# Kernel optimization log

Measured on AMD Instinct MI355X. Metric: run time of the kernel, lower is better.

The kernel has to match this reference:

```python
import jax, jax.numpy as jnp
import numpy as np

E, H, O = 300, 256, 2            # embedding_size, hidden_size, output_size
N_SENT, SENT_LEN, CLAIM_LEN = 2048, 64, 64


def setup_inputs() -> dict:
    key = jax.random.key(0)
    ks = jax.random.split(key, 24)
    rn = lambda k, shape, s=0.05: (jax.random.normal(k, shape, jnp.float32) * s)
    return {
        "claim": jax.random.normal(ks[0], (CLAIM_LEN, E), jnp.float32),
        "sentences": jax.random.normal(ks[1], (N_SENT, SENT_LEN, E), jnp.float32),
        # claim GRU (PyTorch layout: W_ih (3H,E), W_hh (3H,H), gates ordered r,z,n)
        "Wih_c": rn(ks[2], (3 * H, E)), "Whh_c": rn(ks[3], (3 * H, H)),
        "bih_c": rn(ks[4], (3 * H,)), "bhh_c": rn(ks[5], (3 * H,)),
        # sentence GRU
        "Wih_s": rn(ks[6], (3 * H, E)), "Whh_s": rn(ks[7], (3 * H, H)),
        "bih_s": rn(ks[8], (3 * H,)), "bhh_s": rn(ks[9], (3 * H,)),
        # gates (no bias)
        "Wg_s": rn(ks[10], (1, H)), "Wg_c": rn(ks[11], (1, H)),
        # coherence attention
        "Wac": rn(ks[12], (H, H)), "bac": rn(ks[13], (H,)),
        "Was": rn(ks[14], (1, H)), "bas": rn(ks[15], (1,)),
        # extension linear (H, 2H)
        "Wext": rn(ks[16], (H, 2 * H)), "bext": rn(ks[17], (H,)),
        # joint linear (H, 4H), no bias
        "Wj": rn(ks[18], (H, 4 * H)),
        # entailment attention
        "Wae": rn(ks[19], (1, H)), "bae": rn(ks[20], (1,)),
        # final classifier
        "Wf": rn(ks[21], (O, H)), "bf": rn(ks[22], (O,)),
    }


def _gru_last(x, Wih, Whh, bih, bhh):
    """x: (T, B, E) -> final hidden state (B, H). PyTorch GRU math, zero init."""
    B = x.shape[1]
    Hd = Whh.shape[1]
    gi = jnp.einsum('tbe,ge->tbg', x, Wih) + bih  # (T, B, 3H), input projections

    def step(h, gi_t):
        gh = h @ Whh.T + bhh
        ir, iz, inn = jnp.split(gi_t, 3, axis=-1)
        hr, hz, hn = jnp.split(gh, 3, axis=-1)
        r = jax.nn.sigmoid(ir + hr)
        z = jax.nn.sigmoid(iz + hz)
        n = jnp.tanh(inn + r * hn)
        return (1.0 - z) * n + z * h, None

    h0 = jnp.zeros((B, Hd), x.dtype)
    hT, _ = jax.lax.scan(step, h0, gi)
    return hT


def reference(claim, sentences, Wih_c, Whh_c, bih_c, bhh_c,
              Wih_s, Whh_s, bih_s, bhh_s, Wg_s, Wg_c,
              Wac, bac, Was, bas, Wext, bext, Wj, Wae, bae, Wf, bf):
    # claim encoder: (T,1,E) -> hc (1,H)
    hc = _gru_last(claim[:, None, :], Wih_c, Whh_c, bih_c, bhh_c)
    # batched sentence encoder (replaces the per-sentence Python loop)
    HS = _gru_last(jnp.transpose(sentences, (1, 0, 2)), Wih_s, Whh_s, bih_s, bhh_s)  # (N,H)
    # gated fusion of sentence reps with claim rep
    g = jax.nn.sigmoid(HS @ Wg_s.T + hc @ Wg_c.T)          # (N,1)
    HSg = g * HS + (1.0 - g) * hc                           # (N,H)
    # coherence attention over sentences (row-wise softmax)
    scores = (HSg @ Wac.T + bac) @ HSg.T + (HSg @ Was.T + bas)  # (N,N)
    coh = jax.nn.softmax(scores, axis=1)
    H_apo = coh @ HSg                                       # (N,H)
    H_tilde = jnp.tanh(jnp.concatenate([HS, H_apo], axis=1) @ Wext.T + bext)  # (N,H)
    # joint claim-sentence entailment features (replaces per-row loop)
    hc_b = jnp.broadcast_to(hc, H_tilde.shape)
    joint_in = jnp.concatenate(
        [hc_b, H_tilde, hc * H_tilde, jnp.abs(hc - H_tilde)], axis=1)  # (N,4H)
    H_c_s = jnp.tanh(joint_in @ Wj.T)                       # (N,H)
    # entailment attention (softmax over sentence axis)
    ae = jnp.tanh(H_c_s @ Wae.T + bae)                      # (N,1)
    w = jax.nn.softmax(ae, axis=0)                          # (N,1)
    h_c_S = w.T @ H_c_s                                     # (1,H)
    return jax.nn.sigmoid(h_c_S @ Wf.T + bf)                # (1,O)
```

## Files before the change

### kernel.cpp

```cpp
#include <hip/hip_runtime.h>

typedef unsigned short u16;
typedef unsigned int u32;
typedef short bf16x8 __attribute__((ext_vector_type(8)));
typedef float f32x4 __attribute__((ext_vector_type(4)));
typedef u16 u16x4v __attribute__((ext_vector_type(4)));

__device__ __forceinline__ float b2f(u16 h){ return __uint_as_float(((unsigned)h)<<16); }
__device__ __forceinline__ u16 f2b(float f){
  unsigned u = __float_as_uint(f);
  u += 0x7fffu + ((u>>16)&1u);
  return (u16)(u>>16);
}
__device__ __forceinline__ float sigm(float x){ return 1.f/(1.f+__expf(-x)); }
__device__ __forceinline__ float tanh_(float x){
  float ax=fabsf(x), e=__expf(-2.f*ax), t=(1.f-e)/(1.f+e);
  return x<0.f? -t : t;
}
__device__ __forceinline__ bf16x8 ld8a(const u16* p){
  union{ u16x4v h[2]; bf16x8 v; } u;
  u.h[0]=*(const u16x4v*)p; u.h[1]=*(const u16x4v*)(p+4); return u.v;
}
__device__ __forceinline__ f32x4 mfma16(bf16x8 a, bf16x8 b, f32x4 c){
  return __builtin_amdgcn_mfma_f32_16x16x32_bf16(a,b,c,0,0,0);
}

__device__ __forceinline__ void gl_lds16(const void* g, void* s){
  __builtin_amdgcn_global_load_lds(
      (const __attribute__((address_space(1))) void*)g,
      (__attribute__((address_space(3))) void*)s, 16, 0, 0);
}

__device__ __forceinline__ void stage_rows(const u16* base, int ld, int kc,
                                           u16* buf, int w, int l){
  #pragma unroll
  for (int ii=0; ii<6; ii++){
    const int i   = w + ii*8;
    const int row = i*16 + (l>>2);
    const int c8  = (l&3) ^ ((row>>2)&3);
    gl_lds16(base + (long)row*ld + kc*32 + c8*8, buf + i*512);
  }
}
__device__ __forceinline__ bf16x8 ldB(const u16* buf, int row, int l){
  const int slot = (l>>4) ^ ((row>>2)&3);
  return *(const bf16x8*)((const char*)buf + row*64 + slot*16);
}

__global__ __launch_bounds__(256) void cvt_kernel(
    const float* __restrict__ WihS, const float* __restrict__ WhhS,
    const float* __restrict__ WihC, const float* __restrict__ WhhC,
    const float* __restrict__ Wac,  const float* __restrict__ Wext,
    const float* __restrict__ Wj,
    const float* __restrict__ bihS, const float* __restrict__ bhhS,
    const float* __restrict__ bihC, const float* __restrict__ bhhC,
    u16* __restrict__ WihP, u16* __restrict__ WhhSb,
    u16* __restrict__ WihCP, u16* __restrict__ WhhCb,
    u16* __restrict__ WacB, u16* __restrict__ WextB, u16* __restrict__ WjB,
    float* __restrict__ biasGI, float* __restrict__ biasGIC)
{
  const int seg = blockIdx.y;
  int n;
  switch(seg){
    case 0: n = 768*320; break;  case 1: n = 196608; break;
    case 2: n = 768*320; break;  case 3: n = 196608; break;
    case 4: n = 65536; break;    case 5: n = 131072; break;
    case 6: n = 262144; break;   default: n = 1536; break;
  }
  for (int i = blockIdx.x*256 + threadIdx.x; i < n; i += gridDim.x*256){
    switch(seg){
      case 0: { int r=i/320, c=i-r*320; WihP[i]  = (c<300)? f2b(WihS[r*300+c]) : (u16)0; } break;
      case 1: WhhSb[i] = f2b(WhhS[i]); break;
      case 2: { int r=i/320, c=i-r*320; WihCP[i] = (c<300)? f2b(WihC[r*300+c]) : (u16)0; } break;
      case 3: WhhCb[i] = f2b(WhhC[i]); break;
      case 4: WacB[i]  = f2b(Wac[i]);  break;
      case 5: WextB[i] = f2b(Wext[i]); break;
      case 6: WjB[i]   = f2b(Wj[i]);   break;
      default:
        if (i < 768) biasGI[i] = bihS[i] + (i < 512 ? bhhS[i] : 0.f);
        else { int j = i - 768; biasGIC[j] = bihC[j] + (j < 512 ? bhhC[j] : 0.f); }
        break;
    }
  }
}

__global__ __launch_bounds__(512) void gi_kernel(
    const int pass,
    const float* __restrict__ sents, const float* __restrict__ claim,
    const u16* __restrict__ WihP, const float* __restrict__ biasGI,
    const u16* __restrict__ WihCP, const float* __restrict__ biasGIC,
    u16* __restrict__ gi_b, float* __restrict__ giC)
{
  __shared__ __align__(16) u16 SA[64*320];
  __shared__ __align__(16) u16 BB[2][768*32];
  const int tid=threadIdx.x, w=tid>>6, l=tid&63, ar=l&15, kg8=(l>>4)*8;
  const f32x4 z4 = {0.f,0.f,0.f,0.f};
  const bool isClaim = (blockIdx.x == 1024);
  const int b = blockIdx.x;

  for (int i=tid; i<64*80; i+=512){
    int r = i/80, q = i - r*80;
    u16x4v o;
    if (q < 75){
      float4 v;
      if (!isClaim) v = ((const float4*)sents)[(long)(2*b + (r>>5))*4800 + (pass*32 + (r&31))*75 + q];
      else          v = ((const float4*)claim)[r*75 + q];
      o[0]=f2b(v.x); o[1]=f2b(v.y); o[2]=f2b(v.z); o[3]=f2b(v.w);
    } else { o[0]=0; o[1]=0; o[2]=0; o[3]=0; }
    int byte = r*640 + q*8; byte ^= (r&7)<<4;
    *(u16x4v*)((char*)SA + byte) = o;
  }
  const u16* Bw = isClaim ? WihCP : WihP;
  stage_rows(Bw, 320, 0, BB[0], w, l);
  __syncthreads();

  f32x4 acc[24];
  #pragma unroll
  for (int q=0;q<24;q++) acc[q]=z4;

  int cur = 0;
  #pragma unroll
  for (int kc=0;kc<10;kc++){
    if (kc < 9) stage_rows(Bw, 320, kc+1, BB[cur^1], w, l);
    bf16x8 bq[6];
    #pragma unroll
    for (int q=0;q<6;q++) bq[q] = ldB(BB[cur], w*96 + q*16 + ar, l);
    #pragma unroll
    for (int m=0;m<4;m++){
      const int abyte = ((m*16+ar)*640 + (kc*32+kg8)*2) ^ ((ar&7)<<4);
      const bf16x8 a = *(const bf16x8*)((const char*)SA + abyte);
      #pragma unroll
      for (int q=0;q<6;q++) acc[m*6+q] = mfma16(a, bq[q], acc[m*6+q]);
    }
    __syncthreads();
    cur ^= 1;
  }
  const int rb = (l>>4)*4;
  if (!isClaim){
    #pragma unroll
    for (int q=0;q<6;q++){
      const int c = w*96 + q*16 + ar;
      const float bs = biasGI[c];
      #pragma unroll
      for (int m=0;m<4;m++)
        #pragma unroll
        for (int p=0;p<4;p++)
          gi_b[(long)(b*64 + m*16 + rb + p)*768 + c] = f2b(acc[m*6+q][p] + bs);
    }
  } else {
    #pragma unroll
    for (int q=0;q<6;q++){
      const int c = w*96 + q*16 + ar;
      const float bs = biasGIC[c];
      #pragma unroll
      for (int m=0;m<4;m++)
        #pragma unroll
        for (int p=0;p<4;p++)
          giC[(m*16 + rb + p)*768 + c] = acc[m*6+q][p] + bs;
    }
  }
}

__global__ __launch_bounds__(512) void rec_kernel(
    const int pass,
    const u16* __restrict__ gi_b, const u16* __restrict__ WhhSb,
    const float* __restrict__ bhhS,
    float* __restrict__ Hmid, u16* __restrict__ HSout,
    const float* __restrict__ giC, const u16* __restrict__ WhhCb,
    const float* __restrict__ bhhC, const float* __restrict__ Wj,
    const float* __restrict__ WgC,
    float* __restrict__ hcMid, float* __restrict__ hcf,
    float* __restrict__ cvec, float* __restrict__ c0p)
{
  __shared__ __align__(16) u16 Hb[2][16][256];
  __shared__ __align__(16) u16 giL[2][8][776];
  __shared__ __align__(16) u16 WB[2][768*32];
  __shared__ float ghL[768];
  __shared__ float hfL[256];
  __shared__ __align__(16) u16 hbL[256];
  const int tid=threadIdx.x, w=tid>>6, l=tid&63, ar=l&15, kg8=(l>>4)*8;
  const f32x4 z4 = {0.f,0.f,0.f,0.f};

  if (blockIdx.x != 0){
    const long i0 = (long)(blockIdx.x - 1)*8;
    const int rb = (l>>4)*4;
    const float bhn0 = bhhS[512 + w*32 +  0 + ar];
    const float bhn1 = bhhS[512 + w*32 + 16 + ar];

    for (int i=tid; i<2*16*256; i+=512) ((u16*)Hb)[i] = 0;
    __syncthreads();
    float hold[2][4];
    #pragma unroll
    for (int ti=0;ti<2;ti++)
      #pragma unroll
      for (int p=0;p<4;p++) hold[ti][p] = 0.f;
    if (pass==1 && l<32){
      #pragma unroll
      for (int ti=0;ti<2;ti++){
        #pragma unroll
        for (int p=0;p<4;p++){
          const int c = w*32 + ti*16 + ar, rr = rb + p;
          const float h = Hmid[(i0+rr)*256 + c];
          hold[ti][p] = h;
          const int byte = (rr*512 + c*2) ^ ((rr&7)<<4);
          *(u16*)((char*)&Hb[0][0][0] + byte) = f2b(h);
        }
      }
    }
    const u32* g32 = (const u32*)gi_b;
    u32 pf[6];
    #pragma unroll
    for (int rep=0;rep<6;rep++){
      const int i = rep*512 + tid, j = i/384, cu = i - j*384;
      pf[rep] = g32[((i0+j)*32 + 0)*384 + cu];
    }
    #pragma unroll
    for (int rep=0;rep<6;rep++){
      const int i = rep*512 + tid, j = i/384, cu = i - j*384;
      *(u32*)((char*)&giL[0][0][0] + j*1552 + cu*4) = pf[rep];
    }
    stage_rows(WhhSb, 256, 0, WB[0], w, l);
    __syncthreads();

    int cur = 0, kb = 0;
    for (int tl=0; tl<32; tl++){
      const int tn = (tl<31) ? tl+1 : 31;
      #pragma unroll
      for (int rep=0;rep<6;rep++){
        const int i = rep*512 + tid, j = i/384, cu = i - j*384;
        pf[rep] = g32[((i0+j)*32 + tn)*384 + cu];
      }
      f32x4 acc[6];
      #pragma unroll
      for (int q=0;q<6;q++) acc[q]=z4;
      if (l < 32){
        #pragma unroll
        for (int s=0;s<2;s++)
          #pragma unroll
          for (int ti=0;ti<2;ti++)
            #pragma unroll
            for (int p=0;p<4;p++){
              const int c = w*32 + ti*16 + ar;
              const u16 v = *(const u16*)((const char*)&giL[cur][0][0] + (rb+p)*1552 + (s*256+c)*2);
              acc[s*2+ti][p] = b2f(v);
            }
      }
      #pragma unroll
      for (int kc=0;kc<8;kc++){
        const int nkc = (kc<7) ? kc+1 : 0;
        stage_rows(WhhSb, 256, nkc, WB[kb^1], w, l);
        const int abyte = (ar*512 + (kc*32+kg8)*2) ^ ((ar&7)<<4);
        const bf16x8 a = *(const bf16x8*)((const char*)&Hb[cur][0][0] + abyte);
        bf16x8 wq[6];
        #pragma unroll
        for (int s=0;s<3;s++)
          #pragma unroll
          for (int ti=0;ti<2;ti++)
            wq[s*2+ti] = ldB(WB[kb], s*256 + w*32 + ti*16 + ar, l);
        #pragma unroll
        for (int q=0;q<6;q++) acc[q] = mfma16(a, wq[q], acc[q]);
        __syncthreads();
        kb ^= 1;
      }
      #pragma unroll
      for (int rep=0;rep<6;rep++){
        const int i = rep*512 + tid, j = i/384, cu = i - j*384;
        *(u32*)((char*)&giL[cur^1][0][0] + j*1552 + cu*4) = pf[rep];
      }
      if (l < 32){
        #pragma unroll
        for (int ti=0;ti<2;ti++){
          const int c = w*32 + ti*16 + ar;
          const float bhn = ti ? bhn1 : bhn0;
          #pragma unroll
          for (int p=0;p<4;p++){
            const int rr = rb + p;
            const u16 gv = *(const u16*)((const char*)&giL[cur][0][0] + rr*1552 + (512+c)*2);
            const float r_ = sigm(acc[0+ti][p]);
            const float z_ = sigm(acc[2+ti][p]);
            const float n_ = tanh_(b2f(gv) + r_*(acc[4+ti][p] + bhn));
            const float h = (1.f - z_)*n_ + z_*hold[ti][p];
            hold[ti][p] = h;
            const int byte = (rr*512 + c*2) ^ ((rr&7)<<4);
            *(u16*)((char*)&Hb[cur^1][0][0] + byte) = f2b(h);
          }
        }
      }
      __syncthreads();
      cur ^= 1;
    }
    if (l < 32){
      #pragma unroll
      for (int ti=0;ti<2;ti++){
        #pragma unroll
        for (int p=0;p<4;p++){
          const int c = w*32 + ti*16 + ar, rr = rb + p;
          if (pass==0) Hmid[(i0+rr)*256 + c] = hold[ti][p];
          else         HSout[(i0+rr)*512 + c] = f2b(hold[ti][p]);
        }
      }
    }
  } else {
    const u16* wrow[6];
    #pragma unroll
    for (int q=0;q<6;q++) wrow[q] = WhhCb + (w*96 + q*16 + ar)*256 + kg8;
    if (tid < 256){
      const float h0 = (pass==0) ? 0.f : hcMid[tid];
      hfL[tid] = h0; hbL[tid] = f2b(h0);
    }
    __syncthreads();
    for (int tl=0; tl<32; tl++){
      const int t = pass*32 + tl;
      f32x4 a6[6];
      #pragma unroll
      for (int q=0;q<6;q++) a6[q]=z4;
      #pragma unroll
      for (int kc=0;kc<8;kc++){
        bf16x8 wq[6];
        #pragma unroll
        for (int q=0;q<6;q++) wq[q] = ld8a(wrow[q] + kc*32);
        const bf16x8 a = ld8a((const u16*)hbL + kc*32 + kg8);
        #pragma unroll
        for (int q=0;q<6;q++) a6[q] = mfma16(a, wq[q], a6[q]);
      }
      if (l < 16){
        #pragma unroll
        for (int q=0;q<6;q++) ghL[w*96 + q*16 + l] = a6[q][0];
      }
      __syncthreads();
      if (tid < 256){
        const int c = tid;
        const float r_ = sigm(giC[t*768 +       c] + ghL[c]);
        const float z_ = sigm(giC[t*768 + 256 + c] + ghL[256 + c]);
        const float n_ = tanh_(giC[t*768 + 512 + c] + r_*(ghL[512 + c] + bhhC[512 + c]));
        const float h = (1.f - z_)*n_ + z_*hfL[c];
        hfL[c] = h; hbL[c] = f2b(h);
      }
      __syncthreads();
    }
    if (tid < 256){
      const int c = tid;
      const float hv = hfL[c];
      if (pass == 0) hcMid[c] = hv;
      else {
        hcf[c] = hv;
        float acc2 = 0.f;
        for (int k=0;k<256;k++) acc2 += hfL[k]*Wj[(long)c*1024 + k];
        cvec[c] = acc2;
        if (c==0){ float s=0.f; for (int k=0;k<256;k++) s += hfL[k]*WgC[k]; *c0p = s; }
      }
    }
  }
}

__global__ __launch_bounds__(256) void fusion_kernel(
    const u16* __restrict__ HSH, const float* __restrict__ Wgs,
    const float* __restrict__ hcf, const float* __restrict__ c0p,
    u16* __restrict__ HSg, u16* __restrict__ HSgT)
{
  __shared__ float gbuf[64];
  __shared__ __align__(16) u16 tile[64][258];
  const int tid=threadIdx.x, w=tid>>6, l=tid&63;
  const long i0 = (long)blockIdx.x * 64;
  const float c0 = *c0p;
  for (int rr=0; rr<16; rr++){
    long i = i0 + w*16 + rr;
    float p = 0.f;
    for (int c=l; c<256; c+=64) p += b2f(HSH[i*512+c]) * Wgs[c];
    for (int o=32;o;o>>=1) p += __shfl_down(p,o,64);
    if (l==0) gbuf[w*16+rr] = sigm(p + c0);
  }
  __syncthreads();
  for (int idx=tid; idx<64*256; idx+=256){
    int r = idx>>8, c = idx&255;
    float g = gbuf[r];
    float hs = b2f(HSH[(i0+r)*512 + c]);
    u16 bv = f2b(g*hs + (1.f-g)*hcf[c]);
    HSg[(i0+r)*256 + c] = bv;
    tile[r][c] = bv;
  }
  __syncthreads();
  const int ioff = tid&63, cg = tid>>6;
  for (int cc=cg; cc<256; cc+=4)
    HSgT[(long)cc*2048 + i0 + ioff] = tile[ioff][cc];
}

template<int MODE>
__global__ __launch_bounds__(256) void gemmk(
    const u16* __restrict__ A, long lda,
    const u16* __restrict__ Bw, long ldb,
    void* __restrict__ Cp, long ldc, int K,
    const float* __restrict__ biasf,
    const float* __restrict__ hc)
{
  const int tid=threadIdx.x, w=tid>>6, l=tid&63, ar=l&15, kg8=(l>>4)*8;
  const long row0 = (long)blockIdx.x*64 + w*16;
  const long col0 = (long)blockIdx.y*64;
  const f32x4 z4 = {0.f,0.f,0.f,0.f};
  f32x4 acc[4] = {z4,z4,z4,z4};
  const u16* ap = A + (row0+ar)*lda + kg8;
  const u16* bp0 = Bw + (col0+ 0+ar)*ldb + kg8;
  const u16* bp1 = Bw + (col0+16+ar)*ldb + kg8;
  const u16* bp2 = Bw + (col0+32+ar)*ldb + kg8;
  const u16* bp3 = Bw + (col0+48+ar)*ldb + kg8;
  for (int k0=0; k0<K; k0+=32){
    bf16x8 a = ld8a(ap + k0);
    acc[0] = mfma16(a, ld8a(bp0+k0), acc[0]);
    acc[1] = mfma16(a, ld8a(bp1+k0), acc[1]);
    acc[2] = mfma16(a, ld8a(bp2+k0), acc[2]);
    acc[3] = mfma16(a, ld8a(bp3+k0), acc[3]);
  }
  const int rbase = (l>>4)*4;
  #pragma unroll
  for (int t=0;t<4;t++){
    long c = col0 + t*16 + ar;
    #pragma unroll
    for (int p=0;p<4;p++){
      long r = row0 + rbase + p;
      float v = acc[t][p];
      if constexpr (MODE==0){
        if (biasf) v += biasf[c];
        ((u16*)Cp)[r*ldc + c] = f2b(v);
      } else if constexpr (MODE==1){
        ((float*)Cp)[r*ldc + c] = v;
      } else if constexpr (MODE==2){
        float tv = tanh_(v + biasf[c]);
        u16* Uo = (u16*)Cp;
        float hv = hc[c];
        Uo[r*768 + c]       = f2b(tv);
        Uo[r*768 + 256 + c] = f2b(hv*tv);
        Uo[r*768 + 512 + c] = f2b(fabsf(hv - tv));
      } else {
        float tv = tanh_(v + biasf[c]);
        ((u16*)Cp)[r*ldc + c] = f2b(tv);
      }
    }
  }
}

__global__ __launch_bounds__(256) void softmax_rows(float* __restrict__ S)
{
  __shared__ float buf[2048];
  __shared__ float red[4];
  const long i = blockIdx.x;
  float* row = S + i*2048;
  const int tid = threadIdx.x;
  float m = -1e30f;
  for (int c=tid; c<2048; c+=256){ float v=row[c]; buf[c]=v; m=fmaxf(m,v); }
  for (int o=32;o;o>>=1) m = fmaxf(m, __shfl_down(m,o,64));
  if ((tid&63)==0) red[tid>>6] = m;
  __syncthreads();
  m = fmaxf(fmaxf(red[0],red[1]), fmaxf(red[2],red[3]));
  __syncthreads();
  float s = 0.f;
  for (int c=tid; c<2048; c+=256){ float e=__expf(buf[c]-m); buf[c]=e; s+=e; }
  for (int o=32;o;o>>=1) s += __shfl_down(s,o,64);
  if ((tid&63)==0) red[tid>>6] = s;
  __syncthreads();
  s = red[0]+red[1]+red[2]+red[3];
  const float rinv = 1.f/s;
  u16* P = (u16*)S + i*4096;
  for (int c=tid; c<2048; c+=256) P[c] = f2b(buf[c]*rinv);
}

__global__ __launch_bounds__(256) void ae_kernel(
    const u16* __restrict__ Hcs, const float* __restrict__ Wae, const float* __restrict__ bae,
    float* __restrict__ part, float* __restrict__ psum)
{
  __shared__ float aebuf[64];
  const int b=blockIdx.x, tid=threadIdx.x, w=tid>>6, l=tid&63;
  const long i0 = (long)b*64;
  const float baev = bae[0];
  for (int rr=0; rr<16; rr++){
    long i = i0 + w*16 + rr;
    float p = 0.f;
    for (int c=l; c<256; c+=64) p += b2f(Hcs[i*256+c]) * Wae[c];
    for (int o=32;o;o>>=1) p += __shfl_down(p,o,64);
    if (l==0) aebuf[w*16+rr] = __expf(tanh_(p + baev));
  }
  __syncthreads();
  float acc = 0.f;
  const int c = tid;
  for (int r=0;r<64;r++) acc += aebuf[r] * b2f(Hcs[(i0+r)*256 + c]);
  part[b*256 + c] = acc;
  if (tid==0){ float s=0.f; for (int r=0;r<64;r++) s+=aebuf[r]; psum[b]=s; }
}

__global__ __launch_bounds__(256) void final_kernel(
    const float* __restrict__ part, const float* __restrict__ psum,
    const float* __restrict__ Wf, const float* __restrict__ bf_, float* __restrict__ out)
{
  __shared__ float hbuf[256];
  __shared__ float ssum;
  const int tid = threadIdx.x;
  float v = 0.f;
  for (int b=0;b<32;b++) v += part[b*256 + tid];
  hbuf[tid] = v;
  if (tid==0){ float s=0.f; for (int b=0;b<32;b++) s+=psum[b]; ssum=s; }
  __syncthreads();
  const int w = tid>>6, l = tid&63;
  if (w < 2){
    float rinv = 1.f/ssum;
    float p = 0.f;
    for (int c=l; c<256; c+=64) p += hbuf[c]*rinv*Wf[w*256 + c];
    for (int o=32;o;o>>=1) p += __shfl_down(p,o,64);
    if (l==0) out[w] = sigm(p + bf_[w]);
  }
}

extern "C" void kernel_launch(void* const* d_in, const int* in_sizes, int n_in,
                              void* d_out, int out_size, void* d_ws, size_t ws_size,
                              hipStream_t stream)
{
  const float* claim=(const float*)d_in[0];
  const float* sents=(const float*)d_in[1];
  const float* WihC =(const float*)d_in[2];
  const float* WhhC =(const float*)d_in[3];
  const float* bihC =(const float*)d_in[4];
  const float* bhhC =(const float*)d_in[5];
  const float* WihS =(const float*)d_in[6];
  const float* WhhS =(const float*)d_in[7];
  const float* bihS =(const float*)d_in[8];
  const float* bhhS =(const float*)d_in[9];
  const float* WgS  =(const float*)d_in[10];
  const float* WgC  =(const float*)d_in[11];
  const float* Wac  =(const float*)d_in[12];
  const float* bac  =(const float*)d_in[13];
  const float* Wext =(const float*)d_in[16];
  const float* bext =(const float*)d_in[17];
  const float* Wj   =(const float*)d_in[18];
  const float* Wae  =(const float*)d_in[19];
  const float* bae  =(const float*)d_in[20];
  const float* Wf   =(const float*)d_in[21];
  const float* bf_  =(const float*)d_in[22];

  char* ws = (char*)d_ws;
  size_t off = 0;
  auto alloc = [&](size_t b)->void*{ void* p = ws + off; off = (off + b + 255) & ~(size_t)255; return p; };
  float* hcf  = (float*)alloc(256*4);
  float* cvec = (float*)alloc(256*4);
  float* c0p  = (float*)alloc(16);
  float* hcMid= (float*)alloc(256*4);
  float* giC  = (float*)alloc((size_t)64*768*4);
  u16* WihP   = (u16*)alloc((size_t)768*320*2);
  u16* WhhSb  = (u16*)alloc((size_t)196608*2);
  u16* WihCP  = (u16*)alloc((size_t)768*320*2);
  u16* WhhCb  = (u16*)alloc((size_t)196608*2);
  u16* WacB   = (u16*)alloc((size_t)65536*2);
  u16* WextB  = (u16*)alloc((size_t)131072*2);
  u16* WjB    = (u16*)alloc((size_t)262144*2);
  float* biasGI  = (float*)alloc(768*4);
  float* biasGIC = (float*)alloc(768*4);
  u16* HSH  = (u16*)alloc((size_t)2048*512*2);
  u16* HSg  = (u16*)alloc((size_t)2048*256*2);
  u16* HSgT = (u16*)alloc((size_t)256*2048*2);
  u16* A1   = (u16*)alloc((size_t)2048*256*2);
  u16* Up   = (u16*)alloc((size_t)2048*768*2);
  u16* Hcs  = (u16*)alloc((size_t)2048*256*2);
  float* part = (float*)alloc(32*256*4);
  float* psum = (float*)alloc(32*4);
  float* Hmid = (float*)alloc((size_t)2048*256*4);
  u16* gi_b   = (u16*)alloc((size_t)65536*768*2);
  float* S    = (float*)gi_b;

  cvt_kernel<<<dim3(960,8),256,0,stream>>>(WihS,WhhS,WihC,WhhC,Wac,Wext,Wj,
                                           bihS,bhhS,bihC,bhhC,
                                           WihP,WhhSb,WihCP,WhhCb,WacB,WextB,WjB,
                                           biasGI,biasGIC);
  gi_kernel<<<1025,512,0,stream>>>(0,sents,claim,WihP,biasGI,WihCP,biasGIC,gi_b,giC);
  rec_kernel<<<257,512,0,stream>>>(0,gi_b,WhhSb,bhhS,Hmid,HSH,
                                   giC,WhhCb,bhhC,Wj,WgC,hcMid,hcf,cvec,c0p);
  gi_kernel<<<1024,512,0,stream>>>(1,sents,claim,WihP,biasGI,WihCP,biasGIC,gi_b,giC);
  rec_kernel<<<257,512,0,stream>>>(1,gi_b,WhhSb,bhhS,Hmid,HSH,
                                   giC,WhhCb,bhhC,Wj,WgC,hcMid,hcf,cvec,c0p);

  fusion_kernel<<<32,256,0,stream>>>(HSH,WgS,hcf,c0p,HSg,HSgT);
  gemmk<0><<<dim3(32,4),256,0,stream>>>(HSg,256L,WacB,256L,(void*)A1,256L,256,bac,nullptr);
  gemmk<1><<<dim3(32,32),256,0,stream>>>(A1,256L,HSg,256L,(void*)S,2048L,256,nullptr,nullptr);
  softmax_rows<<<2048,256,0,stream>>>(S);
  gemmk<0><<<dim3(32,4),256,0,stream>>>((const u16*)S,4096L,HSgT,2048L,(void*)(HSH+256),512L,2048,nullptr,nullptr);
  gemmk<2><<<dim3(32,4),256,0,stream>>>(HSH,512L,WextB,512L,(void*)Up,768L,512,bext,hcf);
  gemmk<3><<<dim3(32,4),256,0,stream>>>(Up,768L,WjB+256,1024L,(void*)Hcs,256L,768,cvec,nullptr);
  ae_kernel<<<32,256,0,stream>>>(Hcs,Wae,bae,part,psum);
  final_kernel<<<1,256,0,stream>>>(part,psum,Wf,bf_,(float*)d_out);
}
```

Measured before the change: 960.0 us.

## Keep part of Whh in registers and deepen async LDS staging pipeline

The recurrent kernel now holds the first two K-chunks of the sentence Whh in registers for the whole time loop and streams only the remaining six chunks through double-buffered LDS. Waits use explicit vmcnt counts and raw barriers, so global-to-LDS loads stay in flight across chunks. The input-projection GEMM prefetches two chunks ahead under the same scheme, and the claim-path scratch arrays are aliased onto the weight buffer to save LDS. The aim is to cut per-timestep global weight traffic and barrier stalls in the serial recurrence, at the cost of higher register pressure and hand-counted waitcnt values that are fragile to get right.

```diff
diff --git a/kernel.cpp b/kernel.cpp
--- a/kernel.cpp
+++ b/kernel.cpp
@@ -24,6 +24,13 @@
 __device__ __forceinline__ f32x4 mfma16(bf16x8 a, bf16x8 b, f32x4 c){
   return __builtin_amdgcn_mfma_f32_16x16x32_bf16(a,b,c,0,0,0);
 }
+
+#define VMW(N)  do{ asm volatile("s_waitcnt vmcnt(" #N ")" ::: "memory"); \
+                    __builtin_amdgcn_sched_barrier(0); }while(0)
+#define LGK0    do{ asm volatile("s_waitcnt lgkmcnt(0)" ::: "memory"); \
+                    __builtin_amdgcn_sched_barrier(0); }while(0)
+#define BAR()   do{ asm volatile("" ::: "memory"); __builtin_amdgcn_s_barrier(); \
+                    asm volatile("" ::: "memory"); __builtin_amdgcn_sched_barrier(0); }while(0)
 
 __device__ __forceinline__ void gl_lds16(const void* g, void* s){
   __builtin_amdgcn_global_load_lds(
@@ -111,19 +118,21 @@
   }
   const u16* Bw = isClaim ? WihCP : WihP;
   stage_rows(Bw, 320, 0, BB[0], w, l);
-  __syncthreads();
+  stage_rows(Bw, 320, 1, BB[1], w, l);
+  LGK0;
+  BAR();
 
   f32x4 acc[24];
   #pragma unroll
   for (int q=0;q<24;q++) acc[q]=z4;
 
-  int cur = 0;
   #pragma unroll
   for (int kc=0;kc<10;kc++){
-    if (kc < 9) stage_rows(Bw, 320, kc+1, BB[cur^1], w, l);
+    if (kc==9) VMW(0); else VMW(6);
+    BAR();
     bf16x8 bq[6];
     #pragma unroll
-    for (int q=0;q<6;q++) bq[q] = ldB(BB[cur], w*96 + q*16 + ar, l);
+    for (int q=0;q<6;q++) bq[q] = ldB(BB[kc&1], w*96 + q*16 + ar, l);
     #pragma unroll
     for (int m=0;m<4;m++){
       const int abyte = ((m*16+ar)*640 + (kc*32+kg8)*2) ^ ((ar&7)<<4);
@@ -131,9 +140,10 @@
       #pragma unroll
       for (int q=0;q<6;q++) acc[m*6+q] = mfma16(a, bq[q], acc[m*6+q]);
     }
-    __syncthreads();
-    cur ^= 1;
-  }
+    BAR();
+    if (kc<8) stage_rows(Bw, 320, kc+2, BB[kc&1], w, l);
+  }
+  VMW(0);
   const int rb = (l>>4)*4;
   if (!isClaim){
     #pragma unroll
@@ -173,16 +183,24 @@
 {
   __shared__ __align__(16) u16 Hb[2][16][256];
   __shared__ __align__(16) u16 giL[2][8][776];
-  __shared__ __align__(16) u16 WB[2][768*32];
-  __shared__ float ghL[768];
-  __shared__ float hfL[256];
-  __shared__ __align__(16) u16 hbL[256];
+  __shared__ __align__(16) u16 WBd[2][768*32];
   const int tid=threadIdx.x, w=tid>>6, l=tid&63, ar=l&15, kg8=(l>>4)*8;
   const f32x4 z4 = {0.f,0.f,0.f,0.f};
+  float* ghL = (float*)&WBd[0][0];
+  float* hfL = ghL + 768;
+  u16*   hbL = (u16*)(hfL + 256);
 
   if (blockIdx.x != 0){
     const long i0 = (long)(blockIdx.x - 1)*8;
     const int rb = (l>>4)*4;
+    bf16x8 wf[12];
+    #pragma unroll
+    for (int kcR=0;kcR<2;kcR++)
+      #pragma unroll
+      for (int s=0;s<3;s++)
+        #pragma unroll
+        for (int ti=0;ti<2;ti++)
+          wf[kcR*6 + s*2+ti] = ld8a(WhhSb + (s*256 + w*32 + ti*16 + ar)*256 + kcR*32 + kg8);
     const float bhn0 = bhhS[512 + w*32 +  0 + ar];
     const float bhn1 = bhhS[512 + w*32 + 16 + ar];
 
@@ -218,17 +236,23 @@
       const int i = rep*512 + tid, j = i/384, cu = i - j*384;
       *(u32*)((char*)&giL[0][0][0] + j*1552 + cu*4) = pf[rep];
     }
-    stage_rows(WhhSb, 256, 0, WB[0], w, l);
+    stage_rows(WhhSb, 256, 2, WBd[0], w, l);
+    stage_rows(WhhSb, 256, 3, WBd[1], w, l);
     __syncthreads();
 
-    int cur = 0, kb = 0;
+#define MFMA_STREAM(J, BUF) do{ \
+    const int abyte_ = (ar*512 + ((J)*32+kg8)*2) ^ ((ar&7)<<4); \
+    const bf16x8 a_ = *(const bf16x8*)((const char*)&Hb[cur][0][0] + abyte_); \
+    bf16x8 wq_[6]; \
+    _Pragma("unroll") for (int s_=0;s_<3;s_++) \
+    _Pragma("unroll") for (int ti_=0;ti_<2;ti_++) \
+      wq_[s_*2+ti_] = ldB(BUF, s_*256 + w*32 + ti_*16 + ar, l); \
+    _Pragma("unroll") for (int q_=0;q_<6;q_++) acc[q_] = mfma16(a_, wq_[q_], acc[q_]); \
+  }while(0)
+
+    int cur = 0;
     for (int tl=0; tl<32; tl++){
       const int tn = (tl<31) ? tl+1 : 31;
-      #pragma unroll
-      for (int rep=0;rep<6;rep++){
-        const int i = rep*512 + tid, j = i/384, cu = i - j*384;
-        pf[rep] = g32[((i0+j)*32 + tn)*384 + cu];
-      }
       f32x4 acc[6];
       #pragma unroll
       for (int q=0;q<6;q++) acc[q]=z4;
@@ -245,22 +269,29 @@
             }
       }
       #pragma unroll
-      for (int kc=0;kc<8;kc++){
-        const int nkc = (kc<7) ? kc+1 : 0;
-        stage_rows(WhhSb, 256, nkc, WB[kb^1], w, l);
-        const int abyte = (ar*512 + (kc*32+kg8)*2) ^ ((ar&7)<<4);
+      for (int kcR=0;kcR<2;kcR++){
+        const int abyte = (ar*512 + (kcR*32+kg8)*2) ^ ((ar&7)<<4);
         const bf16x8 a = *(const bf16x8*)((const char*)&Hb[cur][0][0] + abyte);
-        bf16x8 wq[6];
-        #pragma unroll
-        for (int s=0;s<3;s++)
-          #pragma unroll
-          for (int ti=0;ti<2;ti++)
-            wq[s*2+ti] = ldB(WB[kb], s*256 + w*32 + ti*16 + ar, l);
-        #pragma unroll
-        for (int q=0;q<6;q++) acc[q] = mfma16(a, wq[q], acc[q]);
-        __syncthreads();
-        kb ^= 1;
-      }
+        #pragma unroll
+        for (int q=0;q<6;q++) acc[q] = mfma16(a, wf[kcR*6+q], acc[q]);
+      }
+      VMW(6);  BAR(); MFMA_STREAM(2, WBd[0]); BAR();
+      stage_rows(WhhSb, 256, 4, WBd[0], w, l);
+      VMW(6);  BAR(); MFMA_STREAM(3, WBd[1]); BAR();
+      stage_rows(WhhSb, 256, 5, WBd[1], w, l);
+      #pragma unroll
+      for (int rep=0;rep<6;rep++){
+        const int i = rep*512 + tid, j = i/384, cu = i - j*384;
+        pf[rep] = g32[((i0+j)*32 + tn)*384 + cu];
+      }
+      VMW(12); BAR(); MFMA_STREAM(4, WBd[0]); BAR();
+      stage_rows(WhhSb, 256, 6, WBd[0], w, l);
+      VMW(12); BAR(); MFMA_STREAM(5, WBd[1]); BAR();
+      stage_rows(WhhSb, 256, 7, WBd[1], w, l);
+      VMW(6);  BAR(); MFMA_STREAM(6, WBd[0]); BAR();
+      stage_rows(WhhSb, 256, 2, WBd[0], w, l);
+      VMW(6);  BAR(); MFMA_STREAM(7, WBd[1]); BAR();
+      stage_rows(WhhSb, 256, 3, WBd[1], w, l);
       #pragma unroll
       for (int rep=0;rep<6;rep++){
         const int i = rep*512 + tid, j = i/384, cu = i - j*384;
@@ -285,9 +316,11 @@
           }
         }
       }
-      __syncthreads();
+      LGK0;
+      BAR();
       cur ^= 1;
     }
+    VMW(0);
     if (l < 32){
       #pragma unroll
       for (int ti=0;ti<2;ti++){
@@ -299,6 +332,7 @@
         }
       }
     }
+#undef MFMA_STREAM
   } else {
     const u16* wrow[6];
     #pragma unroll
```

Result: faster. 869.1 us (-9.5%).

## Read recurrent weights directly from global and deepen input-projection prefetch

Applied to the files above, without the earlier changes.

In the recurrence kernel, W_hh fragments are now loaded straight from global memory (L2-resident) into registers per k-chunk. This replaces staging them through a double-buffered LDS tile with a barrier per chunk, removing eight block-wide syncs per timestep and about 96KB of LDS. In the input-projection kernel, weight staging becomes a two-deep prefetch with explicit vmcnt waits and raw barriers instead of __syncthreads. The trade-off is higher global/L2 load latency on the serial critical path of the recurrence, and more fragile manual wait counting.

```diff
diff --git a/kernel.cpp b/kernel.cpp
--- a/kernel.cpp
+++ b/kernel.cpp
@@ -5,6 +5,7 @@
 typedef short bf16x8 __attribute__((ext_vector_type(8)));
 typedef float f32x4 __attribute__((ext_vector_type(4)));
 typedef u16 u16x4v __attribute__((ext_vector_type(4)));
+typedef u16 u16x8v __attribute__((ext_vector_type(8)));
 
 __device__ __forceinline__ float b2f(u16 h){ return __uint_as_float(((unsigned)h)<<16); }
 __device__ __forceinline__ u16 f2b(float f){
@@ -18,19 +19,24 @@
   return x<0.f? -t : t;
 }
 __device__ __forceinline__ bf16x8 ld8a(const u16* p){
-  union{ u16x4v h[2]; bf16x8 v; } u;
-  u.h[0]=*(const u16x4v*)p; u.h[1]=*(const u16x4v*)(p+4); return u.v;
+  union{ u16x8v h; bf16x8 v; } u; u.h = *(const u16x8v*)p; return u.v;
 }
 __device__ __forceinline__ f32x4 mfma16(bf16x8 a, bf16x8 b, f32x4 c){
   return __builtin_amdgcn_mfma_f32_16x16x32_bf16(a,b,c,0,0,0);
 }
+
+#define VMW(N)  do{ asm volatile("s_waitcnt vmcnt(" #N ")" ::: "memory"); \
+                    __builtin_amdgcn_sched_barrier(0); }while(0)
+#define LGK0    do{ asm volatile("s_waitcnt lgkmcnt(0)" ::: "memory"); \
+                    __builtin_amdgcn_sched_barrier(0); }while(0)
+#define BAR()   do{ asm volatile("" ::: "memory"); __builtin_amdgcn_s_barrier(); \
+                    asm volatile("" ::: "memory"); __builtin_amdgcn_sched_barrier(0); }while(0)
 
 __device__ __forceinline__ void gl_lds16(const void* g, void* s){
   __builtin_amdgcn_global_load_lds(
       (const __attribute__((address_space(1))) void*)g,
       (__attribute__((address_space(3))) void*)s, 16, 0, 0);
 }
-
 __device__ __forceinline__ void stage_rows(const u16* base, int ld, int kc,
                                            u16* buf, int w, int l){
   #pragma unroll
@@ -111,19 +117,21 @@
   }
   const u16* Bw = isClaim ? WihCP : WihP;
   stage_rows(Bw, 320, 0, BB[0], w, l);
-  __syncthreads();
+  stage_rows(Bw, 320, 1, BB[1], w, l);
+  LGK0;
+  BAR();
 
   f32x4 acc[24];
   #pragma unroll
   for (int q=0;q<24;q++) acc[q]=z4;
 
-  int cur = 0;
   #pragma unroll
   for (int kc=0;kc<10;kc++){
-    if (kc < 9) stage_rows(Bw, 320, kc+1, BB[cur^1], w, l);
+    if (kc==9) VMW(0); else VMW(6);
+    BAR();
     bf16x8 bq[6];
     #pragma unroll
-    for (int q=0;q<6;q++) bq[q] = ldB(BB[cur], w*96 + q*16 + ar, l);
+    for (int q=0;q<6;q++) bq[q] = ldB(BB[kc&1], w*96 + q*16 + ar, l);
     #pragma unroll
     for (int m=0;m<4;m++){
       const int abyte = ((m*16+ar)*640 + (kc*32+kg8)*2) ^ ((ar&7)<<4);
@@ -131,9 +139,10 @@
       #pragma unroll
       for (int q=0;q<6;q++) acc[m*6+q] = mfma16(a, bq[q], acc[m*6+q]);
     }
-    __syncthreads();
-    cur ^= 1;
-  }
+    BAR();
+    if (kc<8) stage_rows(Bw, 320, kc+2, BB[kc&1], w, l);
+  }
+  VMW(0);
   const int rb = (l>>4)*4;
   if (!isClaim){
     #pragma unroll
@@ -173,7 +182,6 @@
 {
   __shared__ __align__(16) u16 Hb[2][16][256];
   __shared__ __align__(16) u16 giL[2][8][776];
-  __shared__ __align__(16) u16 WB[2][768*32];
   __shared__ float ghL[768];
   __shared__ float hfL[256];
   __shared__ __align__(16) u16 hbL[256];
@@ -183,6 +191,12 @@
   if (blockIdx.x != 0){
     const long i0 = (long)(blockIdx.x - 1)*8;
     const int rb = (l>>4)*4;
+    const u16* wrow[6];
+    #pragma unroll
+    for (int s=0;s<3;s++)
+      #pragma unroll
+      for (int ti=0;ti<2;ti++)
+        wrow[s*2+ti] = WhhSb + (s*256 + w*32 + ti*16 + ar)*256 + kg8;
     const float bhn0 = bhhS[512 + w*32 +  0 + ar];
     const float bhn1 = bhhS[512 + w*32 + 16 + ar];
 
@@ -218,10 +232,9 @@
       const int i = rep*512 + tid, j = i/384, cu = i - j*384;
       *(u32*)((char*)&giL[0][0][0] + j*1552 + cu*4) = pf[rep];
     }
-    stage_rows(WhhSb, 256, 0, WB[0], w, l);
     __syncthreads();
 
-    int cur = 0, kb = 0;
+    int cur = 0;
     for (int tl=0; tl<32; tl++){
       const int tn = (tl<31) ? tl+1 : 31;
       #pragma unroll
@@ -246,20 +259,13 @@
       }
       #pragma unroll
       for (int kc=0;kc<8;kc++){
-        const int nkc = (kc<7) ? kc+1 : 0;
-        stage_rows(WhhSb, 256, nkc, WB[kb^1], w, l);
+        bf16x8 wq[6];
+        #pragma unroll
+        for (int q=0;q<6;q++) wq[q] = ld8a(wrow[q] + kc*32);
         const int abyte = (ar*512 + (kc*32+kg8)*2) ^ ((ar&7)<<4);
         const bf16x8 a = *(const bf16x8*)((const char*)&Hb[cur][0][0] + abyte);
-        bf16x8 wq[6];
-        #pragma unroll
-        for (int s=0;s<3;s++)
-          #pragma unroll
-          for (int ti=0;ti<2;ti++)
-            wq[s*2+ti] = ldB(WB[kb], s*256 + w*32 + ti*16 + ar, l);
         #pragma unroll
         for (int q=0;q<6;q++) acc[q] = mfma16(a, wq[q], acc[q]);
-        __syncthreads();
-        kb ^= 1;
       }
       #pragma unroll
       for (int rep=0;rep<6;rep++){
```

Measured after the change: 922.1 us. 1.04x faster.
